# Kernel optimization log

Measured on AMD Instinct MI355X. Metric: run time of the kernel, lower is better.

Reference implementation:

```python
import jax, jax.numpy as jnp
import numpy as np

B, IN_DIM, H, OUT_DIM = 2048, 1024, 256, 512   # batch, input_dim, hidden_dim, output_dim
T, K, HOPS = 12, 3, 4                            # num_tempers, ops per temper, max_path_hops


def setup_inputs() -> dict:
    key = jax.random.key(0)
    ks = jax.random.split(key, 10)
    s = 0.02
    return dict(
        x=jax.random.normal(ks[0], (B, IN_DIM), jnp.float32),
        init_tempers=jax.random.randint(ks[1], (B,), 0, T),
        op_noise=jax.random.normal(ks[2], (HOPS, T, K), jnp.float32),
        route_u=jax.random.uniform(ks[3], (HOPS, B, T + 1), jnp.float32),
        W_in=jax.random.normal(ks[4], (IN_DIM, H), jnp.float32) * s,
        b_in=jnp.zeros((H,), jnp.float32),
        W1=jax.random.normal(ks[5], (T, K, H, H), jnp.float32) * s,
        b1=jnp.zeros((T, K, H), jnp.float32),
        W2=jax.random.normal(ks[6], (T, K, H, H), jnp.float32) * s,
        b2=jnp.zeros((T, K, H), jnp.float32),
        Wr=jax.random.normal(ks[7], (T, H, T + 1), jnp.float32) * s,
        br=jnp.zeros((T, T + 1), jnp.float32),
        W_out=jax.random.normal(ks[8], (H, OUT_DIM), jnp.float32) * s,
        b_out=jnp.zeros((OUT_DIM,), jnp.float32),
    )


def reference(x, init_tempers, op_noise, route_u, W_in, b_in, W1, b1, W2, b2, Wr, br, W_out, b_out):
    # input projection; num_patches = hidden//hidden = 1, so patches == x_proj [N, H]
    states = x @ W_in + b_in                      # [N, H]
    N = states.shape[0]
    tempers = init_tempers                        # [N] in [0, T)
    done = jnp.zeros((N,), dtype=bool)

    for hop in range(HOPS):
        # per-temper operator mixing weights: softmax over randn(3) per Temper call
        w = jax.nn.softmax(op_noise[hop], axis=-1)                      # [T, K]
        # run all T expert MLPs densely (static-shape MoE dispatch), combine via one-hot
        h1 = jax.nn.relu(jnp.einsum('nh,tkhd->tnkd', states, W1) + b1[:, None])   # [T, N, K, H]
        h2 = jax.nn.relu(jnp.einsum('tnkd,tkdf->tnkf', h1, W2) + b2[:, None])     # [T, N, K, H]
        out_t = jnp.einsum('tnkf,tk->tnf', h2, w)                                  # [T, N, H]
        logits_t = jnp.einsum('tnf,tfg->tng', out_t, Wr) + br[:, None]             # [T, N, T+1]
        sel = jax.nn.one_hot(tempers, T, dtype=states.dtype)                       # [N, T]
        out = jnp.einsum('tnf,nt->nf', out_t, sel)                                 # [N, H]
        logits = jnp.einsum('tng,nt->ng', logits_t, sel)                           # [N, T+1]
        # multinomial(softmax(logits)) == argmax(logits + Gumbel)
        g = -jnp.log(-jnp.log(route_u[hop] + 1e-9) + 1e-9)
        sampled = jnp.argmax(logits + g, axis=-1)                                  # [N]
        active = ~done
        states = jnp.where(active[:, None], out, states)
        tempers = jnp.where(active, jnp.minimum(sampled, T - 1), tempers)
        done = done | (active & (sampled == T))

    # view(B, 1, H).mean(dim=1) is identity since num_patches == 1
    return states @ W_out + b_out
```

## Files before the change

### kernel.cpp

```cpp
#include <hip/hip_runtime.h>
#include <math.h>

#define BN_   2048
#define INDIM 1024
#define HD    256
#define OD    512
#define TN    12
#define KN    3
#define NHOPS 4
#define TP1   13

#define ER    8
#define CR    16

__device__ __forceinline__ void gll16(const float* g, float* l) {
  __builtin_amdgcn_global_load_lds(
      (const __attribute__((address_space(1))) void*)g,
      (__attribute__((address_space(3))) void*)l, 16, 0, 0);
}

__device__ __forceinline__ float4 ld4(const float* p) { return *(const float4*)p; }

__device__ __forceinline__ void fma4(float4& c, float a, const float4 b) {
  c.x = fmaf(a, b.x, c.x); c.y = fmaf(a, b.y, c.y);
  c.z = fmaf(a, b.z, c.z); c.w = fmaf(a, b.w, c.w);
}
__device__ __forceinline__ void add4(float4& c, const float4 b) {
  c.x += b.x; c.y += b.y; c.z += b.z; c.w += b.w;
}

template<int NR>
__device__ __forceinline__ void kloop2(float4* acc, const float* SA, int astr,
                                       const float* w0, int ws, int nk4, int ks0) {
  const float* wp = w0;
  float4 a0 = ld4(wp),          a1 = ld4(wp + ws),
         a2 = ld4(wp + 2 * ws), a3 = ld4(wp + 3 * ws);
  float4 b0 = ld4(wp + 4 * ws), b1 = ld4(wp + 5 * ws),
         b2 = ld4(wp + 6 * ws), b3 = ld4(wp + 7 * ws);
#pragma unroll 1
  for (int k4 = 0; k4 < nk4 - 2; k4 += 2) {
    float4 c0 = ld4(wp + 8 * ws),  c1 = ld4(wp + 9 * ws),
           c2 = ld4(wp + 10 * ws), c3 = ld4(wp + 11 * ws);
    const int kk = ks0 + k4 * 4;
#pragma unroll
    for (int r = 0; r < NR; ++r) {
      float4 av = *(const float4*)(SA + r * astr + kk);
      fma4(acc[r], av.x, a0); fma4(acc[r], av.y, a1);
      fma4(acc[r], av.z, a2); fma4(acc[r], av.w, a3);
    }
    float4 d0 = ld4(wp + 12 * ws), d1 = ld4(wp + 13 * ws),
           d2 = ld4(wp + 14 * ws), d3 = ld4(wp + 15 * ws);
#pragma unroll
    for (int r = 0; r < NR; ++r) {
      float4 av = *(const float4*)(SA + r * astr + kk + 4);
      fma4(acc[r], av.x, b0); fma4(acc[r], av.y, b1);
      fma4(acc[r], av.z, b2); fma4(acc[r], av.w, b3);
    }
    a0 = c0; a1 = c1; a2 = c2; a3 = c3;
    b0 = d0; b1 = d1; b2 = d2; b3 = d3;
    wp += 8 * ws;
  }
  const int kk = ks0 + (nk4 - 2) * 4;
#pragma unroll
  for (int r = 0; r < NR; ++r) {
    float4 av = *(const float4*)(SA + r * astr + kk);
    fma4(acc[r], av.x, a0); fma4(acc[r], av.y, a1);
    fma4(acc[r], av.z, a2); fma4(acc[r], av.w, a3);
  }
#pragma unroll
  for (int r = 0; r < NR; ++r) {
    float4 av = *(const float4*)(SA + r * astr + kk + 4);
    fma4(acc[r], av.x, b0); fma4(acc[r], av.y, b1);
    fma4(acc[r], av.z, b2); fma4(acc[r], av.w, b3);
  }
}

template<int NR>
__device__ __forceinline__ void reduce4(float4* acc, float4 (*pbA)[64],
                                        float4 (*pbB)[64], int w, int tx) {
  __syncthreads();
  if (w == 1) {
#pragma unroll
    for (int r = 0; r < NR; ++r) pbA[r][tx] = acc[r];
  } else if (w == 3) {
#pragma unroll
    for (int r = 0; r < NR; ++r) pbB[r][tx] = acc[r];
  }
  __syncthreads();
  if (w == 0) {
#pragma unroll
    for (int r = 0; r < NR; ++r) add4(acc[r], pbA[r][tx]);
  } else if (w == 2) {
#pragma unroll
    for (int r = 0; r < NR; ++r) add4(acc[r], pbB[r][tx]);
  }
  __syncthreads();
  if (w == 2) {
#pragma unroll
    for (int r = 0; r < NR; ++r) pbA[r][tx] = acc[r];
  }
  __syncthreads();
  if (w == 0) {
#pragma unroll
    for (int r = 0; r < NR; ++r) add4(acc[r], pbA[r][tx]);
  }
}

__global__ __launch_bounds__(1024) void k_init(const int* __restrict__ init_t,
                                               int* __restrict__ cnt,
                                               int* __restrict__ gidx) {
  const int tid = threadIdx.x;
  if (tid < NHOPS * 16) cnt[tid] = 0;
  __syncthreads();
  for (int n = tid; n < BN_; n += 1024) {
    int t = init_t[n];
    int slot = atomicAdd(&cnt[t], 1);
    gidx[t * BN_ + slot] = n;
  }
}

__global__ __launch_bounds__(256) void k_gemm_in(const float* __restrict__ A,
                                                 const float* __restrict__ W,
                                                 float* __restrict__ pp) {
  const int bm = blockIdx.x * ER;
  const int kh = blockIdx.y;
  __shared__ float  sA[ER][512];
  __shared__ float4 pbA[ER][64];
  __shared__ float4 pbB[ER][64];
  const int tid = threadIdx.x;
  const int tx = tid & 63;
  const int w = tid >> 6;

#pragma unroll
  for (int l = 0; l < 4; ++l) {
    int idx = tid + l * 256;
    int r = idx >> 7;
    int c = (idx & 127) << 2;
    gll16(&A[(size_t)(bm + r) * INDIM + kh * 512 + c], &sA[r][c]);
  }
  __syncthreads();

  float4 acc[ER];
#pragma unroll
  for (int r = 0; r < ER; ++r) acc[r] = make_float4(0.f, 0.f, 0.f, 0.f);

  const int ks = w * 128;
  kloop2<ER>(acc, &sA[0][0], 512, W + (size_t)(kh * 512 + ks) * HD + tx * 4, HD, 32, ks);
  reduce4<ER>(acc, pbA, pbB, w, tx);

  if (w == 0) {
#pragma unroll
    for (int r = 0; r < ER; ++r)
      *(float4*)&pp[((size_t)kh * BN_ + bm + r) * HD + tx * 4] = acc[r];
  }
}

__global__ __launch_bounds__(256) void k_cin(const float* __restrict__ pp,
                                             const float* __restrict__ bias,
                                             float* __restrict__ states) {
  int idx = blockIdx.x * 256 + threadIdx.x;
  int c = (idx & 63) << 2;
  float4 a = ld4(&pp[(size_t)idx * 4]);
  float4 b = ld4(&pp[(size_t)BN_ * HD + (size_t)idx * 4]);
  float4 bv = ld4(&bias[c]);
  float4 o = make_float4(a.x + b.x + bv.x, a.y + b.y + bv.y,
                         a.z + b.z + bv.z, a.w + b.w + bv.w);
  *(float4*)&states[(size_t)idx * 4] = o;
}

__global__ __launch_bounds__(256) void k_gemm_out(const float* __restrict__ A,
                                                  const float* __restrict__ W,
                                                  const float* __restrict__ bias,
                                                  float* __restrict__ C) {
  const int bm = blockIdx.x * ER;
  const int cb = blockIdx.y * 256;
  __shared__ float  sA[ER][HD];
  __shared__ float4 pbA[ER][64];
  __shared__ float4 pbB[ER][64];
  const int tid = threadIdx.x;
  const int tx = tid & 63;
  const int w = tid >> 6;

#pragma unroll
  for (int l = 0; l < 2; ++l) {
    int idx = tid + l * 256;
    int r = idx >> 6;
    int c = (idx & 63) << 2;
    gll16(&A[(size_t)(bm + r) * HD + c], &sA[r][c]);
  }
  __syncthreads();

  float4 acc[ER];
#pragma unroll
  for (int r = 0; r < ER; ++r) acc[r] = make_float4(0.f, 0.f, 0.f, 0.f);

  const int ks = w * 64;
  kloop2<ER>(acc, &sA[0][0], HD, W + (size_t)ks * OD + cb + tx * 4, OD, 16, ks);
  reduce4<ER>(acc, pbA, pbB, w, tx);

  if (w == 0) {
    float4 bv = ld4(&bias[cb + tx * 4]);
#pragma unroll
    for (int r = 0; r < ER; ++r) {
      float4 o = make_float4(acc[r].x + bv.x, acc[r].y + bv.y,
                             acc[r].z + bv.z, acc[r].w + bv.w);
      *(float4*)&C[(size_t)(bm + r) * OD + cb + tx * 4] = o;
    }
  }
}

__global__ __launch_bounds__(256) void k_h1h2(
    int hop,
    const float* __restrict__ W1, const float* __restrict__ b1,
    const float* __restrict__ W2, const float* __restrict__ b2,
    const float* __restrict__ op_noise,
    const int* __restrict__ cnt, const int* __restrict__ gidx,
    const float* __restrict__ states, float* __restrict__ part) {
  const int bid = blockIdx.x;
  const int xcd = bid & 7;
  const int s   = bid >> 3;
  const int u   = xcd * 3 + (s % 3);
  const int inner = s / 3;
  const int k   = inner % 3;
  const int j   = inner / 3;
  const int t   = u >> 1;
  const int h   = u & 1;
  const int rb  = j * 2 + h;

  const int cntv = cnt[hop * 16 + t];
  const int r0 = rb * ER;
  if (r0 >= cntv) return;
  const int gb = (hop * TN + t) * BN_ + r0;
  const int rows = min(ER, cntv - r0);

  __shared__ float  sA[ER][HD];
  __shared__ float  sH[ER][HD];
  __shared__ float4 pbA[ER][64];
  __shared__ float4 pbB[ER][64];
  const int tid = threadIdx.x;
  const int tx = tid & 63;
  const int w = tid >> 6;

#pragma unroll
  for (int l = 0; l < 2; ++l) {
    int r = w + 4 * l;
    int c = tx << 2;
    if (r < rows)
      gll16(&states[(size_t)gidx[gb + r] * HD + c], &sA[r][c]);
  }
  __syncthreads();

  const float* Wa = W1 + (size_t)(t * KN + k) * HD * HD;
  const float* Wb = W2 + (size_t)(t * KN + k) * HD * HD;
  const int ks = w * 64;

  float4 acc[ER];
#pragma unroll
  for (int r = 0; r < ER; ++r) acc[r] = make_float4(0.f, 0.f, 0.f, 0.f);

  kloop2<ER>(acc, &sA[0][0], HD, Wa + (size_t)ks * HD + tx * 4, HD, 16, ks);
  reduce4<ER>(acc, pbA, pbB, w, tx);

  if (w == 0) {
    float4 bv = ld4(&b1[(t * KN + k) * HD + tx * 4]);
#pragma unroll
    for (int r = 0; r < ER; ++r) {
      float4 hh;
      hh.x = fmaxf(acc[r].x + bv.x, 0.f);
      hh.y = fmaxf(acc[r].y + bv.y, 0.f);
      hh.z = fmaxf(acc[r].z + bv.z, 0.f);
      hh.w = fmaxf(acc[r].w + bv.w, 0.f);
      *(float4*)&sH[r][tx * 4] = hh;
    }
  }
  __syncthreads();

#pragma unroll
  for (int r = 0; r < ER; ++r) acc[r] = make_float4(0.f, 0.f, 0.f, 0.f);
  kloop2<ER>(acc, &sH[0][0], HD, Wb + (size_t)ks * HD + tx * 4, HD, 16, ks);
  reduce4<ER>(acc, pbA, pbB, w, tx);

  if (w == 0) {
    float wkk;
    {
      const float* on = op_noise + (hop * TN + t) * KN;
      float x0 = on[0], x1 = on[1], x2 = on[2];
      float m = fmaxf(fmaxf(x0, x1), x2);
      float e0 = expf(x0 - m), e1 = expf(x1 - m), e2 = expf(x2 - m);
      float ek = (k == 0) ? e0 : (k == 1) ? e1 : e2;
      wkk = ek / (e0 + e1 + e2);
    }
    float4 bv = ld4(&b2[(t * KN + k) * HD + tx * 4]);
#pragma unroll
    for (int r = 0; r < ER; ++r) {
      if (r < rows) {
        int n = gidx[gb + r];
        float4 o;
        o.x = wkk * fmaxf(acc[r].x + bv.x, 0.f);
        o.y = wkk * fmaxf(acc[r].y + bv.y, 0.f);
        o.z = wkk * fmaxf(acc[r].z + bv.z, 0.f);
        o.w = wkk * fmaxf(acc[r].w + bv.w, 0.f);
        *(float4*)&part[((size_t)k * BN_ + n) * HD + tx * 4] = o;
      }
    }
  }
}

__global__ __launch_bounds__(256) void k_comb(
    int hop,
    const float* __restrict__ Wr, const float* __restrict__ br,
    const float* __restrict__ route_u,
    int* __restrict__ cnt, int* __restrict__ gidx,
    const float* __restrict__ part,
    float* __restrict__ states) {
  const int t  = blockIdx.x % TN;
  const int rb = blockIdx.x / TN;
  const int cntv = cnt[hop * 16 + t];
  const int r0 = rb * CR;
  if (r0 >= cntv) return;
  const int gb = (hop * TN + t) * BN_ + r0;
  const int rows = min(CR, cntv - r0);

  __shared__ float sO[CR][HD + 4];
  __shared__ float sWr[HD * TP1];
  __shared__ float sL[CR][16];
  __shared__ int   sN[CR];

  const int tid = threadIdx.x;
  if (tid < CR && tid < rows) sN[tid] = gidx[gb + tid];

#pragma unroll
  for (int l = 0; l < 4; ++l) {
    int idx = tid + l * 256;
    int r = idx >> 6;
    int c = (idx & 63) << 2;
    if (r < rows) {
      int n = gidx[gb + r];
      size_t p = (size_t)n * HD + c;
      float4 a = ld4(&part[p]);
      float4 b = ld4(&part[(size_t)BN_ * HD + p]);
      float4 cc = ld4(&part[(size_t)2 * BN_ * HD + p]);
      float4 v = make_float4(a.x + b.x + cc.x, a.y + b.y + cc.y,
                             a.z + b.z + cc.z, a.w + b.w + cc.w);
      *(float4*)&sO[r][c] = v;
      *(float4*)&states[(size_t)n * HD + c] = v;
    }
  }
  for (int i = tid; i < HD * TP1; i += 256)
    sWr[i] = Wr[(size_t)t * HD * TP1 + i];
  __syncthreads();

  int r = tid >> 4, g = tid & 15;
  if (r < rows && g < TP1) {
    float a = br[t * TP1 + g];
#pragma unroll 8
    for (int f = 0; f < HD; ++f) a = fmaf(sO[r][f], sWr[f * TP1 + g], a);
    float u = route_u[((size_t)hop * BN_ + sN[r]) * TP1 + g];
    float gb_ = -logf(-logf(u + 1e-9f) + 1e-9f);
    sL[r][g] = a + gb_;
  }
  __syncthreads();

  if (tid < rows) {
    float best = sL[tid][0];
    int bj = 0;
#pragma unroll
    for (int gg = 1; gg < TP1; ++gg) {
      float v = sL[tid][gg];
      if (v > best) { best = v; bj = gg; }
    }
    if (hop + 1 < NHOPS && bj != TN) {
      int n = sN[tid];
      int slot = atomicAdd(&cnt[(hop + 1) * 16 + bj], 1);
      gidx[((hop + 1) * TN + bj) * BN_ + slot] = n;
    }
  }
}

extern "C" void kernel_launch(void* const* d_in, const int* in_sizes, int n_in,
                              void* d_out, int out_size, void* d_ws, size_t ws_size,
                              hipStream_t stream) {
  const float* x        = (const float*)d_in[0];
  const int*   init_t   = (const int*)d_in[1];
  const float* op_noise = (const float*)d_in[2];
  const float* route_u  = (const float*)d_in[3];
  const float* W_in     = (const float*)d_in[4];
  const float* b_in     = (const float*)d_in[5];
  const float* W1       = (const float*)d_in[6];
  const float* b1       = (const float*)d_in[7];
  const float* W2       = (const float*)d_in[8];
  const float* b2       = (const float*)d_in[9];
  const float* Wr       = (const float*)d_in[10];
  const float* br       = (const float*)d_in[11];
  const float* W_out    = (const float*)d_in[12];
  const float* b_out    = (const float*)d_in[13];
  float* out = (float*)d_out;

  float* states = (float*)d_ws;
  float* part   = states + (size_t)BN_ * HD;
  float* pp     = part;
  int* cnt  = (int*)(part + (size_t)KN * BN_ * HD);
  int* gidx = cnt + NHOPS * 16;

  k_init<<<1, 1024, 0, stream>>>(init_t, cnt, gidx);

  k_gemm_in<<<dim3(BN_ / ER, 2), 256, 0, stream>>>(x, W_in, pp);
  k_cin<<<(BN_ * HD / 4) / 256, 256, 0, stream>>>(pp, b_in, states);

  for (int hop = 0; hop < NHOPS; ++hop) {
    k_h1h2<<<8 * 3 * 3 * 128, 256, 0, stream>>>(
        hop, W1, b1, W2, b2, op_noise, cnt, gidx, states, part);
    k_comb<<<TN * (BN_ / CR), 256, 0, stream>>>(
        hop, Wr, br, route_u, cnt, gidx, part, states);
  }

  k_gemm_out<<<dim3(BN_ / ER, OD / 256), 256, 0, stream>>>(states, W_out, b_out, out);
}
```

Measured before the change: 220.3 us.

## Retile expert MLP kernel to 8 columns per thread with 8-way K split

The k_h1h2 expert MLP kernel now has each thread compute 8 output columns instead of 4, and splits the K dimension eight ways (four waves times two half-waves of 32 rows each) instead of four. The new inner loop register-double-buffers the weight loads and reads 4 K values of activations per LDS access. The cross-slice reduction becomes a multi-step LDS tree that reuses the sA/sH buffers as scratch. This targets weight-load latency and LDS traffic per FMA, at the cost of more registers and extra barriers in the reduction.

```diff
diff --git a/kernel.cpp b/kernel.cpp
--- a/kernel.cpp
+++ b/kernel.cpp
@@ -106,6 +106,81 @@
   }
 }
 
+__device__ __forceinline__ void kloop_hw(float4 (*acc)[2], const float* SA,
+                                         const float* Wbase, int kb, int cg) {
+  const float* wp = Wbase + (size_t)kb * HD + cg * 8;
+  float4 c0[4], c1[4];
+#pragma unroll
+  for (int j = 0; j < 4; ++j) { c0[j] = ld4(wp + j * HD); c1[j] = ld4(wp + j * HD + 4); }
+#pragma unroll 1
+  for (int it = 0; it < 7; ++it) {
+    const float* wn = wp + 4 * HD;
+    float4 n0[4], n1[4];
+#pragma unroll
+    for (int j = 0; j < 4; ++j) { n0[j] = ld4(wn + j * HD); n1[j] = ld4(wn + j * HD + 4); }
+    const int kk = kb + it * 4;
+#pragma unroll
+    for (int r = 0; r < ER; ++r) {
+      float4 av = *(const float4*)(SA + r * HD + kk);
+      fma4(acc[r][0], av.x, c0[0]); fma4(acc[r][1], av.x, c1[0]);
+      fma4(acc[r][0], av.y, c0[1]); fma4(acc[r][1], av.y, c1[1]);
+      fma4(acc[r][0], av.z, c0[2]); fma4(acc[r][1], av.z, c1[2]);
+      fma4(acc[r][0], av.w, c0[3]); fma4(acc[r][1], av.w, c1[3]);
+    }
+#pragma unroll
+    for (int j = 0; j < 4; ++j) { c0[j] = n0[j]; c1[j] = n1[j]; }
+    wp = wn;
+  }
+  const int kk = kb + 28;
+#pragma unroll
+  for (int r = 0; r < ER; ++r) {
+    float4 av = *(const float4*)(SA + r * HD + kk);
+    fma4(acc[r][0], av.x, c0[0]); fma4(acc[r][1], av.x, c1[0]);
+    fma4(acc[r][0], av.y, c0[1]); fma4(acc[r][1], av.y, c1[1]);
+    fma4(acc[r][0], av.z, c0[2]); fma4(acc[r][1], av.z, c1[2]);
+    fma4(acc[r][0], av.w, c0[3]); fma4(acc[r][1], av.w, c1[3]);
+  }
+}
+
+__device__ __forceinline__ void reduce8h(float4 (*acc)[2],
+    float4 (*pbA)[64], float4 (*pbB)[64], float4 (*pbC)[64], float4 (*pbD)[64],
+    int w, int hw, int cg) {
+  __syncthreads();
+  if (hw == 1) {
+    float4 (*dst)[64] = (w == 0) ? pbA : (w == 1) ? pbB : (w == 2) ? pbC : pbD;
+#pragma unroll
+    for (int r = 0; r < ER; ++r) { dst[r][cg * 2] = acc[r][0]; dst[r][cg * 2 + 1] = acc[r][1]; }
+  }
+  __syncthreads();
+  if (hw == 0) {
+    float4 (*src)[64] = (w == 0) ? pbA : (w == 1) ? pbB : (w == 2) ? pbC : pbD;
+#pragma unroll
+    for (int r = 0; r < ER; ++r) { add4(acc[r][0], src[r][cg * 2]); add4(acc[r][1], src[r][cg * 2 + 1]); }
+  }
+  __syncthreads();
+  if (hw == 0 && (w == 1 || w == 3)) {
+    float4 (*dst)[64] = (w == 1) ? pbA : pbB;
+#pragma unroll
+    for (int r = 0; r < ER; ++r) { dst[r][cg * 2] = acc[r][0]; dst[r][cg * 2 + 1] = acc[r][1]; }
+  }
+  __syncthreads();
+  if (hw == 0 && (w == 0 || w == 2)) {
+    float4 (*src)[64] = (w == 0) ? pbA : pbB;
+#pragma unroll
+    for (int r = 0; r < ER; ++r) { add4(acc[r][0], src[r][cg * 2]); add4(acc[r][1], src[r][cg * 2 + 1]); }
+  }
+  __syncthreads();
+  if (hw == 0 && w == 2) {
+#pragma unroll
+    for (int r = 0; r < ER; ++r) { pbA[r][cg * 2] = acc[r][0]; pbA[r][cg * 2 + 1] = acc[r][1]; }
+  }
+  __syncthreads();
+  if (hw == 0 && w == 0) {
+#pragma unroll
+    for (int r = 0; r < ER; ++r) { add4(acc[r][0], pbA[r][cg * 2]); add4(acc[r][1], pbA[r][cg * 2 + 1]); }
+  }
+}
+
 __global__ __launch_bounds__(1024) void k_init(const int* __restrict__ init_t,
                                                int* __restrict__ cnt,
                                                int* __restrict__ gidx) {
@@ -124,7 +199,7 @@
                                                  float* __restrict__ pp) {
   const int bm = blockIdx.x * ER;
   const int kh = blockIdx.y;
-  __shared__ float  sA[ER][512];
+  __shared__ __align__(16) float sA[ER][512];
   __shared__ float4 pbA[ER][64];
   __shared__ float4 pbB[ER][64];
   const int tid = threadIdx.x;
@@ -174,7 +249,7 @@
                                                   float* __restrict__ C) {
   const int bm = blockIdx.x * ER;
   const int cb = blockIdx.y * 256;
-  __shared__ float  sA[ER][HD];
+  __shared__ __align__(16) float sA[ER][HD];
   __shared__ float4 pbA[ER][64];
   __shared__ float4 pbB[ER][64];
   const int tid = threadIdx.x;
@@ -224,8 +299,8 @@
   const int k   = inner % 3;
   const int j   = inner / 3;
   const int t   = u >> 1;
-  const int h   = u & 1;
-  const int rb  = j * 2 + h;
+  const int uh  = u & 1;
+  const int rb  = j * 2 + uh;
 
   const int cntv = cnt[hop * 16 + t];
   const int r0 = rb * ER;
@@ -233,18 +308,22 @@
   const int gb = (hop * TN + t) * BN_ + r0;
   const int rows = min(ER, cntv - r0);
 
-  __shared__ float  sA[ER][HD];
-  __shared__ float  sH[ER][HD];
+  __shared__ __align__(16) float sA[ER][HD];
+  __shared__ __align__(16) float sH[ER][HD];
   __shared__ float4 pbA[ER][64];
   __shared__ float4 pbB[ER][64];
   const int tid = threadIdx.x;
-  const int tx = tid & 63;
-  const int w = tid >> 6;
+  const int w  = tid >> 6;
+  const int hw = (tid >> 5) & 1;
+  const int cg = tid & 31;
+  const int kb = w * 64 + hw * 32;
+  float4 (*pbC)[64] = (float4 (*)[64])sA;
+  float4 (*pbD)[64] = (float4 (*)[64])sH;
 
 #pragma unroll
   for (int l = 0; l < 2; ++l) {
     int r = w + 4 * l;
-    int c = tx << 2;
+    int c = (tid & 63) << 2;
     if (r < rows)
       gll16(&states[(size_t)gidx[gb + r] * HD + c], &sA[r][c]);
   }
@@ -252,35 +331,47 @@
 
   const float* Wa = W1 + (size_t)(t * KN + k) * HD * HD;
   const float* Wb = W2 + (size_t)(t * KN + k) * HD * HD;
-  const int ks = w * 64;
-
-  float4 acc[ER];
-#pragma unroll
-  for (int r = 0; r < ER; ++r) acc[r] = make_float4(0.f, 0.f, 0.f, 0.f);
-
-  kloop2<ER>(acc, &sA[0][0], HD, Wa + (size_t)ks * HD + tx * 4, HD, 16, ks);
-  reduce4<ER>(acc, pbA, pbB, w, tx);
-
-  if (w == 0) {
-    float4 bv = ld4(&b1[(t * KN + k) * HD + tx * 4]);
+
+  float4 acc[ER][2];
+#pragma unroll
+  for (int r = 0; r < ER; ++r) {
+    acc[r][0] = make_float4(0.f, 0.f, 0.f, 0.f);
+    acc[r][1] = make_float4(0.f, 0.f, 0.f, 0.f);
+  }
+
+  kloop_hw(acc, &sA[0][0], Wa, kb, cg);
+  reduce8h(acc, pbA, pbB, pbC, pbD, w, hw, cg);
+
+  if (w == 0 && hw == 0) {
+    const float* ba = b1 + (t * KN + k) * HD;
+    float4 bv0 = ld4(ba + cg * 8);
+    float4 bv1 = ld4(ba + cg * 8 + 4);
 #pragma unroll
     for (int r = 0; r < ER; ++r) {
-      float4 hh;
-      hh.x = fmaxf(acc[r].x + bv.x, 0.f);
-      hh.y = fmaxf(acc[r].y + bv.y, 0.f);
-      hh.z = fmaxf(acc[r].z + bv.z, 0.f);
-      hh.w = fmaxf(acc[r].w + bv.w, 0.f);
-      *(float4*)&sH[r][tx * 4] = hh;
-    }
-  }
-  __syncthreads();
-
-#pragma unroll
-  for (int r = 0; r < ER; ++r) acc[r] = make_float4(0.f, 0.f, 0.f, 0.f);
-  kloop2<ER>(acc, &sH[0][0], HD, Wb + (size_t)ks * HD + tx * 4, HD, 16, ks);
-  reduce4<ER>(acc, pbA, pbB, w, tx);
-
-  if (w == 0) {
+      float4 h0, h1v;
+      h0.x = fmaxf(acc[r][0].x + bv0.x, 0.f);
+      h0.y = fmaxf(acc[r][0].y + bv0.y, 0.f);
+      h0.z = fmaxf(acc[r][0].z + bv0.z, 0.f);
+      h0.w = fmaxf(acc[r][0].w + bv0.w, 0.f);
+      h1v.x = fmaxf(acc[r][1].x + bv1.x, 0.f);
+      h1v.y = fmaxf(acc[r][1].y + bv1.y, 0.f);
+      h1v.z = fmaxf(acc[r][1].z + bv1.z, 0.f);
+      h1v.w = fmaxf(acc[r][1].w + bv1.w, 0.f);
+      *(float4*)&sH[r][cg * 8]     = h0;
+      *(float4*)&sH[r][cg * 8 + 4] = h1v;
+    }
+  }
+  __syncthreads();
+
+#pragma unroll
+  for (int r = 0; r < ER; ++r) {
+    acc[r][0] = make_float4(0.f, 0.f, 0.f, 0.f);
+    acc[r][1] = make_float4(0.f, 0.f, 0.f, 0.f);
+  }
+  kloop_hw(acc, &sH[0][0], Wb, kb, cg);
+  reduce8h(acc, pbA, pbB, pbC, pbD, w, hw, cg);
+
+  if (w == 0 && hw == 0) {
     float wkk;
     {
       const float* on = op_noise + (hop * TN + t) * KN;
@@ -290,17 +381,24 @@
       float ek = (k == 0) ? e0 : (k == 1) ? e1 : e2;
       wkk = ek / (e0 + e1 + e2);
     }
-    float4 bv = ld4(&b2[(t * KN + k) * HD + tx * 4]);
+    const float* bb = b2 + (t * KN + k) * HD;
+    float4 bv0 = ld4(bb + cg * 8);
+    float4 bv1 = ld4(bb + cg * 8 + 4);
 #pragma unroll
     for (int r = 0; r < ER; ++r) {
       if (r < rows) {
         int n = gidx[gb + r];
-        float4 o;
-        o.x = wkk * fmaxf(acc[r].x + bv.x, 0.f);
-        o.y = wkk * fmaxf(acc[r].y + bv.y, 0.f);
-        o.z = wkk * fmaxf(acc[r].z + bv.z, 0.f);
-        o.w = wkk * fmaxf(acc[r].w + bv.w, 0.f);
-        *(float4*)&part[((size_t)k * BN_ + n) * HD + tx * 4] = o;
+        float4 o0, o1;
+        o0.x = wkk * fmaxf(acc[r][0].x + bv0.x, 0.f);
+        o0.y = wkk * fmaxf(acc[r][0].y + bv0.y, 0.f);
+        o0.z = wkk * fmaxf(acc[r][0].z + bv0.z, 0.f);
+        o0.w = wkk * fmaxf(acc[r][0].w + bv0.w, 0.f);
+        o1.x = wkk * fmaxf(acc[r][1].x + bv1.x, 0.f);
+        o1.y = wkk * fmaxf(acc[r][1].y + bv1.y, 0.f);
+        o1.z = wkk * fmaxf(acc[r][1].z + bv1.z, 0.f);
+        o1.w = wkk * fmaxf(acc[r][1].w + bv1.w, 0.f);
+        *(float4*)&part[((size_t)k * BN_ + n) * HD + cg * 8]     = o0;
+        *(float4*)&part[((size_t)k * BN_ + n) * HD + cg * 8 + 4] = o1;
       }
     }
   }
```

Result: slower. 251.4 us (+14.1%).

## Double rows per expert block and reuse reduction buffer for hidden activations

Applied to the files above, without the earlier changes.

Each block of the expert MLP kernel now processes 16 gathered rows instead of 8, so every W1/W2 weight tile loaded from memory is reused across twice as many rows. To fit the larger tiles, the hidden activation buffer aliases the reduction scratch buffer, and the kernel declares an occupancy hint of 3 blocks per CU. The XCD-aware block index swizzle is replaced by a plain linear mapping. The larger register accumulator arrays and the loss of the L2-locality swizzle could lower occupancy or cache hit rate.

```diff
diff --git a/kernel.cpp b/kernel.cpp
--- a/kernel.cpp
+++ b/kernel.cpp
@@ -11,6 +11,7 @@
 #define TP1   13
 
 #define ER    8
+#define EH    16
 #define CR    16
 
 __device__ __forceinline__ void gll16(const float* g, float* l) {
@@ -124,7 +125,7 @@
                                                  float* __restrict__ pp) {
   const int bm = blockIdx.x * ER;
   const int kh = blockIdx.y;
-  __shared__ float  sA[ER][512];
+  __shared__ __align__(16) float sA[ER][512];
   __shared__ float4 pbA[ER][64];
   __shared__ float4 pbB[ER][64];
   const int tid = threadIdx.x;
@@ -174,7 +175,7 @@
                                                   float* __restrict__ C) {
   const int bm = blockIdx.x * ER;
   const int cb = blockIdx.y * 256;
-  __shared__ float  sA[ER][HD];
+  __shared__ __align__(16) float sA[ER][HD];
   __shared__ float4 pbA[ER][64];
   __shared__ float4 pbB[ER][64];
   const int tid = threadIdx.x;
@@ -209,7 +210,7 @@
   }
 }
 
-__global__ __launch_bounds__(256) void k_h1h2(
+__global__ __launch_bounds__(256, 3) void k_h1h2(
     int hop,
     const float* __restrict__ W1, const float* __restrict__ b1,
     const float* __restrict__ W2, const float* __restrict__ b2,
@@ -217,34 +218,29 @@
     const int* __restrict__ cnt, const int* __restrict__ gidx,
     const float* __restrict__ states, float* __restrict__ part) {
   const int bid = blockIdx.x;
-  const int xcd = bid & 7;
-  const int s   = bid >> 3;
-  const int u   = xcd * 3 + (s % 3);
-  const int inner = s / 3;
-  const int k   = inner % 3;
-  const int j   = inner / 3;
-  const int t   = u >> 1;
-  const int h   = u & 1;
-  const int rb  = j * 2 + h;
+  const int t  = bid / (KN * 128);
+  const int k  = (bid / 128) % KN;
+  const int j  = bid & 127;
 
   const int cntv = cnt[hop * 16 + t];
-  const int r0 = rb * ER;
+  const int r0 = j * EH;
   if (r0 >= cntv) return;
   const int gb = (hop * TN + t) * BN_ + r0;
-  const int rows = min(ER, cntv - r0);
-
-  __shared__ float  sA[ER][HD];
-  __shared__ float  sH[ER][HD];
-  __shared__ float4 pbA[ER][64];
-  __shared__ float4 pbB[ER][64];
+  const int rows = min(EH, cntv - r0);
+
+  __shared__ __align__(16) float sA[EH][HD];
+  __shared__ float4 pbA[EH][64];
+  __shared__ float4 pbB[EH][64];
   const int tid = threadIdx.x;
   const int tx = tid & 63;
   const int w = tid >> 6;
-
-#pragma unroll
-  for (int l = 0; l < 2; ++l) {
-    int r = w + 4 * l;
-    int c = tx << 2;
+  float* sH = (float*)pbB;
+
+#pragma unroll
+  for (int l = 0; l < 4; ++l) {
+    int idx = tid + l * 256;
+    int r = idx >> 6;
+    int c = (idx & 63) << 2;
     if (r < rows)
       gll16(&states[(size_t)gidx[gb + r] * HD + c], &sA[r][c]);
   }
@@ -254,31 +250,31 @@
   const float* Wb = W2 + (size_t)(t * KN + k) * HD * HD;
   const int ks = w * 64;
 
-  float4 acc[ER];
-#pragma unroll
-  for (int r = 0; r < ER; ++r) acc[r] = make_float4(0.f, 0.f, 0.f, 0.f);
-
-  kloop2<ER>(acc, &sA[0][0], HD, Wa + (size_t)ks * HD + tx * 4, HD, 16, ks);
-  reduce4<ER>(acc, pbA, pbB, w, tx);
+  float4 acc[EH];
+#pragma unroll
+  for (int r = 0; r < EH; ++r) acc[r] = make_float4(0.f, 0.f, 0.f, 0.f);
+
+  kloop2<EH>(acc, &sA[0][0], HD, Wa + (size_t)ks * HD + tx * 4, HD, 16, ks);
+  reduce4<EH>(acc, pbA, pbB, w, tx);
 
   if (w == 0) {
     float4 bv = ld4(&b1[(t * KN + k) * HD + tx * 4]);
 #pragma unroll
-    for (int r = 0; r < ER; ++r) {
-      float4 hh;
-      hh.x = fmaxf(acc[r].x + bv.x, 0.f);
-      hh.y = fmaxf(acc[r].y + bv.y, 0.f);
-      hh.z = fmaxf(acc[r].z + bv.z, 0.f);
-      hh.w = fmaxf(acc[r].w + bv.w, 0.f);
-      *(float4*)&sH[r][tx * 4] = hh;
-    }
-  }
-  __syncthreads();
-
-#pragma unroll
-  for (int r = 0; r < ER; ++r) acc[r] = make_float4(0.f, 0.f, 0.f, 0.f);
-  kloop2<ER>(acc, &sH[0][0], HD, Wb + (size_t)ks * HD + tx * 4, HD, 16, ks);
-  reduce4<ER>(acc, pbA, pbB, w, tx);
+    for (int r = 0; r < EH; ++r) {
+      float4 h;
+      h.x = fmaxf(acc[r].x + bv.x, 0.f);
+      h.y = fmaxf(acc[r].y + bv.y, 0.f);
+      h.z = fmaxf(acc[r].z + bv.z, 0.f);
+      h.w = fmaxf(acc[r].w + bv.w, 0.f);
+      *(float4*)&sH[r * HD + tx * 4] = h;
+    }
+  }
+  __syncthreads();
+
+#pragma unroll
+  for (int r = 0; r < EH; ++r) acc[r] = make_float4(0.f, 0.f, 0.f, 0.f);
+  kloop2<EH>(acc, sH, HD, Wb + (size_t)ks * HD + tx * 4, HD, 16, ks);
+  reduce4<EH>(acc, pbA, pbB, w, tx);
 
   if (w == 0) {
     float wkk;
@@ -292,7 +288,7 @@
     }
     float4 bv = ld4(&b2[(t * KN + k) * HD + tx * 4]);
 #pragma unroll
-    for (int r = 0; r < ER; ++r) {
+    for (int r = 0; r < EH; ++r) {
       if (r < rows) {
         int n = gidx[gb + r];
         float4 o;
@@ -408,7 +404,7 @@
   k_cin<<<(BN_ * HD / 4) / 256, 256, 0, stream>>>(pp, b_in, states);
 
   for (int hop = 0; hop < NHOPS; ++hop) {
-    k_h1h2<<<8 * 3 * 3 * 128, 256, 0, stream>>>(
+    k_h1h2<<<TN * KN * 128, 256, 0, stream>>>(
         hop, W1, b1, W2, b2, op_noise, cnt, gidx, states, part);
     k_comb<<<TN * (BN_ / CR), 256, 0, stream>>>(
         hop, Wr, br, route_u, cnt, gidx, part, states);
```

Result: slower. 472.2 us (median of 2 runs) (+114.3%).
